# Kernel optimization log

Hardware: AMD Instinct MI355X
Metric: run time of the kernel (lower is better)

Reference implementation:

```python
import jax, jax.numpy as jnp
import numpy as np

EPS = 1e-8
N_ITER = 3
S = 8      # n_slots
D = 64     # slot_size
HID = 128  # mlp hidden


def _ln(x, w, b):
    m = jnp.mean(x, axis=-1, keepdims=True)
    v = jnp.var(x, axis=-1, keepdims=True)
    return (x - m) * jax.lax.rsqrt(v + 1e-5) * w + b


def setup_inputs() -> dict:
    key = jax.random.key(0)
    ks = jax.random.split(key, 20)
    B, N, Din = 128, 4096, 64
    g = lambda k, sh, s: (jax.random.normal(k, sh, jnp.float32) * s)
    return {
        "inputs": jax.random.normal(ks[0], (B, N, Din), jnp.float32),
        "eps_noise": jax.random.normal(ks[1], (B, S, D), jnp.float32),
        "slot_mu": g(ks[2], (1, 1, D), 0.1),
        "slot_logvar": g(ks[3], (1, 1, D), 0.1),
        "k_w": g(ks[4], (D, Din), 1.0 / np.sqrt(Din)),
        "v_w": g(ks[5], (D, Din), 1.0 / np.sqrt(Din)),
        "q_w": g(ks[6], (D, D), 1.0 / np.sqrt(D)),
        "ni_w": jnp.ones((Din,), jnp.float32), "ni_b": jnp.zeros((Din,), jnp.float32),
        "ns_w": jnp.ones((D,), jnp.float32),  "ns_b": jnp.zeros((D,), jnp.float32),
        "nr_w": jnp.ones((D,), jnp.float32),  "nr_b": jnp.zeros((D,), jnp.float32),
        "gru_wih": g(ks[7], (3 * D, D), 1.0 / np.sqrt(D)),
        "gru_whh": g(ks[8], (3 * D, D), 1.0 / np.sqrt(D)),
        "gru_bih": jnp.zeros((3 * D,), jnp.float32),
        "gru_bhh": jnp.zeros((3 * D,), jnp.float32),
        "mlp_w1": g(ks[9], (HID, D), 1.0 / np.sqrt(D)),
        "mlp_w2": g(ks[10], (D, HID), 1.0 / np.sqrt(HID)),
        "mlp_b2": jnp.zeros((D,), jnp.float32),
    }


def _gru(x, h, wih, whh, bih, bhh):
    gi = x @ wih.T + bih  # [BS, 3D]
    gh = h @ whh.T + bhh
    i_r, i_z, i_n = jnp.split(gi, 3, axis=-1)
    h_r, h_z, h_n = jnp.split(gh, 3, axis=-1)
    r = jax.nn.sigmoid(i_r + h_r)
    z = jax.nn.sigmoid(i_z + h_z)
    n = jnp.tanh(i_n + r * h_n)
    return (1.0 - z) * n + z * h


def _step(slots, k, v, q_w, ns_w, ns_b, nr_w, nr_b,
          gru_wih, gru_whh, gru_bih, gru_bhh, mlp_w1, mlp_w2, mlp_b2):
    B = slots.shape[0]
    q = _ln(slots, ns_w, ns_b) @ q_w.T                     # [B,S,D]
    logits = jnp.einsum('bnd,bsd->bns', k, q)              # [B,N,S]
    w = jax.nn.softmax(logits, axis=-1) + EPS              # softmax over slots
    w = w / jnp.sum(w, axis=-2, keepdims=True)             # renorm over tokens
    atten_maps = jnp.einsum('bns,bnd->bsd', w, v)          # [B,S,D]
    h = _gru(atten_maps.reshape(B * S, D), slots.reshape(B * S, D),
             gru_wih, gru_whh, gru_bih, gru_bhh)
    h = h + (jax.nn.relu(_ln(h, nr_w, nr_b) @ mlp_w1.T) @ mlp_w2.T + mlp_b2)
    return h.reshape(B, S, D), w


def reference(inputs, eps_noise, slot_mu, slot_logvar, k_w, v_w, q_w,
              ni_w, ni_b, ns_w, ns_b, nr_w, nr_b,
              gru_wih, gru_whh, gru_bih, gru_bhh, mlp_w1, mlp_w2, mlp_b2):
    std = jnp.exp(0.5 * slot_logvar)
    slots = slot_mu + std * eps_noise                      # [B,S,D]
    x = _ln(inputs, ni_w, ni_b)
    k = (x @ k_w.T) / np.sqrt(D).astype(np.float32)        # [B,N,D]
    v = x @ v_w.T
    args = (q_w, ns_w, ns_b, nr_w, nr_b, gru_wih, gru_whh,
            gru_bih, gru_bhh, mlp_w1, mlp_w2, mlp_b2)
    for _ in range(N_ITER):
        slots, w = _step(slots, k, v, *args)
    slots, w = _step(jax.lax.stop_gradient(slots), k, v, *args)
    return slots, w
```

## Files before the change

kernel.cpp:

```cpp
#include <hip/hip_runtime.h>
#include <hip/hip_bf16.h>

#define BB 128
#define NN 4096
#define DD 64
#define SS 8
#define HH 128

typedef __attribute__((ext_vector_type(8))) short short8;
typedef __attribute__((ext_vector_type(4))) float f32x4;

__device__ __forceinline__ float warp_red_sum(float v) {
    #pragma unroll
    for (int off = 32; off; off >>= 1) v += __shfl_xor(v, off);
    return v;
}

__device__ __forceinline__ float bcastlane(float v, int l) {
    return __int_as_float(__builtin_amdgcn_readlane(__float_as_int(v), l));
}

__device__ __forceinline__ unsigned short bfu(float f) {
    __hip_bfloat16 h = __float2bfloat16(f);
    return *(unsigned short*)&h;
}

__device__ __forceinline__ unsigned pk2(float a, float b) {
    return (unsigned)bfu(a) | ((unsigned)bfu(b) << 16);
}

__global__ __launch_bounds__(256) void prep_kernel(
    const float* __restrict__ k_w, const float* __restrict__ v_w, const float* __restrict__ q_w,
    const float* __restrict__ wih, const float* __restrict__ whh,
    const float* __restrict__ w1, const float* __restrict__ w2,
    unsigned short* __restrict__ wcat, float* __restrict__ qwT,
    float* __restrict__ wihT, float* __restrict__ whhT,
    float* __restrict__ w1T, float* __restrict__ w2T)
{
    int i0 = blockIdx.x * blockDim.x + threadIdx.x;
    int nthr = gridDim.x * blockDim.x;
    for (int t = i0; t < 8192; t += nthr) {
        int n = t >> 6, k = t & 63;
        float val = (n < 64) ? k_w[n * 64 + k] * 0.125f : v_w[(n - 64) * 64 + k];
        wcat[t] = bfu(val);
    }
    for (int t = i0; t < 4096; t += nthr) {
        int r = t >> 6, c = t & 63;
        qwT[t] = q_w[c * 64 + r];
    }
    for (int t = i0; t < 12288; t += nthr) {
        int r = t / 192, c = t % 192;
        wihT[t] = wih[c * 64 + r];
        whhT[t] = whh[c * 64 + r];
    }
    for (int t = i0; t < 8192; t += nthr) {
        int r = t >> 7, c = t & 127;
        w1T[t] = w1[c * 64 + r];
    }
    for (int t = i0; t < 8192; t += nthr) {
        int r = t >> 6, c = t & 63;
        w2T[t] = w2[c * 128 + r];
    }
}

__global__ __launch_bounds__(256) void slots_init_kernel(
    const float* __restrict__ eps, const float* __restrict__ mu,
    const float* __restrict__ lv, float* __restrict__ slots)
{
    int idx = blockIdx.x * blockDim.x + threadIdx.x;
    int d = idx & 63;
    slots[idx] = mu[d] + __expf(0.5f * lv[d]) * eps[idx];
}

__global__ __launch_bounds__(256) void phase_a_mfma(
    const float* __restrict__ inp, const unsigned short* __restrict__ wcat,
    const float* __restrict__ niw, const float* __restrict__ nib,
    unsigned short* __restrict__ kbu, unsigned short* __restrict__ vbt)
{
    __shared__ short smemA[18432];
    short* Xs = smemA;
    short* Ws = smemA + 9216;
    float* tbuf = (float*)smemA;
    const int tid = threadIdx.x, lane = tid & 63, widx = tid >> 6;

    {
        const unsigned* wg = (const unsigned*)wcat;
        #pragma unroll 4
        for (int t = tid; t < 4096; t += 256) {
            int n = t >> 5, kp = t & 31;
            *(unsigned*)&Ws[n * 72 + kp * 2] = wg[t];
        }
    }

    const int tg = lane >> 4, dq = lane & 15;
    const float4 wni = *(const float4*)&niw[dq * 4];
    const float4 bni = *(const float4*)&nib[dq * 4];
    const int tok0 = blockIdx.x * 128;
    #pragma unroll
    for (int it = 0; it < 8; ++it) {
        const int m = widx * 32 + it * 4 + tg;
        float4 x = *(const float4*)&inp[(size_t)(tok0 + m) * 64 + dq * 4];
        float s1 = x.x + x.y + x.z + x.w;
        float s2 = fmaf(x.x, x.x, fmaf(x.y, x.y, fmaf(x.z, x.z, x.w * x.w)));
        #pragma unroll
        for (int o = 1; o < 16; o <<= 1) { s1 += __shfl_xor(s1, o); s2 += __shfl_xor(s2, o); }
        float mean = s1 * (1.0f / 64.0f);
        float var = s2 * (1.0f / 64.0f) - mean * mean;
        float rstd = rsqrtf(var + 1e-5f);
        float y0 = (x.x - mean) * rstd * wni.x + bni.x;
        float y1 = (x.y - mean) * rstd * wni.y + bni.y;
        float y2 = (x.z - mean) * rstd * wni.z + bni.z;
        float y3 = (x.w - mean) * rstd * wni.w + bni.w;
        uint2 p; p.x = pk2(y0, y1); p.y = pk2(y2, y3);
        *(uint2*)&Xs[m * 72 + dq * 4] = p;
    }
    __syncthreads();

    const int quad = lane >> 4, l16 = lane & 15;
    short8 afr[2][2];
    #pragma unroll
    for (int mt = 0; mt < 2; ++mt)
        #pragma unroll
        for (int ks = 0; ks < 2; ++ks)
            afr[mt][ks] = *(const short8*)&Xs[(widx * 32 + mt * 16 + l16) * 72 + ks * 32 + quad * 8];

    f32x4 acc[2][8];
    #pragma unroll
    for (int mt = 0; mt < 2; ++mt)
        #pragma unroll
        for (int nt = 0; nt < 8; ++nt)
            acc[mt][nt] = (f32x4){0.f, 0.f, 0.f, 0.f};

    #pragma unroll
    for (int nt = 0; nt < 8; ++nt) {
        #pragma unroll
        for (int ks = 0; ks < 2; ++ks) {
            short8 bfr = *(const short8*)&Ws[(nt * 16 + l16) * 72 + ks * 32 + quad * 8];
            acc[0][nt] = __builtin_amdgcn_mfma_f32_16x16x32_bf16(afr[0][ks], bfr, acc[0][nt], 0, 0, 0);
            acc[1][nt] = __builtin_amdgcn_mfma_f32_16x16x32_bf16(afr[1][ks], bfr, acc[1][nt], 0, 0, 0);
        }
    }

    __syncthreads();
    #pragma unroll
    for (int mt = 0; mt < 2; ++mt)
        #pragma unroll
        for (int nt = 0; nt < 4; ++nt)
            #pragma unroll
            for (int r = 0; r < 4; ++r)
                tbuf[(widx * 32 + mt * 16 + quad * 4 + r) * 68 + nt * 16 + l16] = acc[mt][nt][r];
    __syncthreads();
    {
        const int row = tid >> 1, half = tid & 1;
        #pragma unroll
        for (int c = 0; c < 4; ++c) {
            float4 f0 = *(float4*)&tbuf[row * 68 + half * 32 + c * 8];
            float4 f1 = *(float4*)&tbuf[row * 68 + half * 32 + c * 8 + 4];
            uint4 o;
            o.x = pk2(f0.x, f0.y); o.y = pk2(f0.z, f0.w);
            o.z = pk2(f1.x, f1.y); o.w = pk2(f1.z, f1.w);
            *(uint4*)&kbu[(size_t)(tok0 + row) * 64 + half * 32 + c * 8] = o;
        }
    }

    __syncthreads();
    #pragma unroll
    for (int mt = 0; mt < 2; ++mt)
        #pragma unroll
        for (int nt = 4; nt < 8; ++nt)
            #pragma unroll
            for (int r = 0; r < 4; ++r)
                tbuf[((nt - 4) * 16 + l16) * 132 + widx * 32 + mt * 16 + quad * 4 + r] = acc[mt][nt][r];
    __syncthreads();
    {
        const int b = blockIdx.x >> 5, tin = (blockIdx.x & 31) * 128;
        const int d = tid >> 2, q4 = tid & 3;
        #pragma unroll
        for (int c = 0; c < 4; ++c) {
            float4 f0 = *(float4*)&tbuf[d * 132 + q4 * 32 + c * 8];
            float4 f1 = *(float4*)&tbuf[d * 132 + q4 * 32 + c * 8 + 4];
            uint4 o;
            o.x = pk2(f0.x, f0.y); o.y = pk2(f0.z, f0.w);
            o.z = pk2(f1.x, f1.y); o.w = pk2(f1.z, f1.w);
            *(uint4*)&vbt[((size_t)b * 64 + d) * 4096 + tin + q4 * 32 + c * 8] = o;
        }
    }
}

__global__ __launch_bounds__(256) void q_kernel(
    const float* __restrict__ slots, const float* __restrict__ qwT,
    const float* __restrict__ nsw, const float* __restrict__ nsb,
    unsigned short* __restrict__ qout)
{
    const int lane = threadIdx.x & 63;
    const int row = blockIdx.x * 4 + (threadIdx.x >> 6);
    float x = slots[row * 64 + lane];
    float m = warp_red_sum(x) * (1.0f / 64.0f);
    float dx = x - m;
    float var = warp_red_sum(dx * dx) * (1.0f / 64.0f);
    float xln = dx * rsqrtf(var + 1e-5f) * nsw[lane] + nsb[lane];
    float acc = 0.f;
    #pragma unroll 16
    for (int i = 0; i < 64; ++i) acc = fmaf(bcastlane(xln, i), qwT[i * 64 + lane], acc);
    qout[row * 64 + lane] = bfu(acc);
}

__global__ __launch_bounds__(256) void attn_mfma(
    const __hip_bfloat16* __restrict__ kb, const unsigned short* __restrict__ vbt,
    const unsigned short* __restrict__ qb,
    float* __restrict__ numer, float* __restrict__ denom, float* __restrict__ wout)
{
    __shared__ unsigned short smem[24192];
    unsigned short* Qs = smem;
    const int tid = threadIdx.x, lane = tid & 63, widx = tid >> 6;
    unsigned short* wls = smem + 1152 + widx * 1152;
    unsigned short* vt  = smem + 5760 + widx * 4608;
    const int b = blockIdx.y;

    for (int t = tid; t < 1024; t += 256) {
        int s = t >> 6, dd = t & 63;
        Qs[s * 72 + dd] = (s < 8) ? qb[b * 512 + t] : (unsigned short)0;
    }
    for (int t = lane; t < 576; t += 64) wls[576 + t] = 0;
    __syncthreads();

    const int quad = lane >> 4, l16 = lane & 15;
    short8 bq0 = *(const short8*)&Qs[l16 * 72 + quad * 8];
    short8 bq1 = *(const short8*)&Qs[l16 * 72 + 32 + quad * 8];

    f32x4 accv[4];
    #pragma unroll
    for (int nt = 0; nt < 4; ++nt) accv[nt] = (f32x4){0.f, 0.f, 0.f, 0.f};
    float dsum = 0.f;

    const int twave0 = blockIdx.x * 512 + widx * 128;
    const int vd = lane >> 3, vc = (lane & 7) * 8;
    #pragma unroll
    for (int iter = 0; iter < 2; ++iter) {
        const int t0 = twave0 + iter * 64;
        uint4 vld[8];
        #pragma unroll
        for (int i = 0; i < 8; ++i)
            vld[i] = *(const uint4*)&vbt[((size_t)b * 64 + i * 8 + vd) * 4096 + t0 + vc];

        #pragma unroll
        for (int t4 = 0; t4 < 4; ++t4) {
            const size_t krow = ((size_t)b * NN + t0 + t4 * 16 + l16) * 64;
            short8 ak0 = *(const short8*)&kb[krow + quad * 8];
            short8 ak1 = *(const short8*)&kb[krow + 32 + quad * 8];
            f32x4 lg = (f32x4){0.f, 0.f, 0.f, 0.f};
            lg = __builtin_amdgcn_mfma_f32_16x16x32_bf16(ak0, bq0, lg, 0, 0, 0);
            lg = __builtin_amdgcn_mfma_f32_16x16x32_bf16(ak1, bq1, lg, 0, 0, 0);
            float wv[4];
            #pragma unroll
            for (int r = 0; r < 4; ++r) {
                float e = __expf(lg[r]);
                float s = e;
                s += __shfl_xor(s, 1); s += __shfl_xor(s, 2); s += __shfl_xor(s, 4);
                wv[r] = e / s + 1e-8f;
                dsum += wv[r];
            }
            if (l16 < 8) {
                *(unsigned*)&wls[l16 * 72 + t4 * 16 + quad * 4]     = pk2(wv[0], wv[1]);
                *(unsigned*)&wls[l16 * 72 + t4 * 16 + quad * 4 + 2] = pk2(wv[2], wv[3]);
                if (wout) {
                    float* wp = wout + ((size_t)b * NN + t0 + t4 * 16 + quad * 4) * 8 + l16;
                    wp[0] = wv[0]; wp[8] = wv[1]; wp[16] = wv[2]; wp[24] = wv[3];
                }
            }
        }
        #pragma unroll
        for (int i = 0; i < 8; ++i)
            *(uint4*)&vt[(i * 8 + vd) * 72 + vc] = vld[i];
        #pragma unroll
        for (int ks = 0; ks < 2; ++ks) {
            short8 aw = *(const short8*)&wls[l16 * 72 + ks * 32 + quad * 8];
            #pragma unroll
            for (int nt = 0; nt < 4; ++nt) {
                short8 bv = *(const short8*)&vt[(nt * 16 + l16) * 72 + ks * 32 + quad * 8];
                accv[nt] = __builtin_amdgcn_mfma_f32_16x16x32_bf16(aw, bv, accv[nt], 0, 0, 0);
            }
        }
    }
    dsum += __shfl_xor(dsum, 16);
    dsum += __shfl_xor(dsum, 32);
    __syncthreads();
    float* red = (float*)(smem + 5760);
    float* dred = red + 2048;
    if (quad < 2) {
        #pragma unroll
        for (int nt = 0; nt < 4; ++nt)
            #pragma unroll
            for (int r = 0; r < 4; ++r)
                red[widx * 512 + (quad * 4 + r) * 64 + nt * 16 + l16] = accv[nt][r];
    }
    if (quad == 0 && l16 < 8) dred[widx * 8 + l16] = dsum;
    __syncthreads();
    for (int e = tid; e < 512; e += 256)
        atomicAdd(numer + (size_t)b * 512 + e, red[e] + red[512 + e] + red[1024 + e] + red[1536 + e]);
    if (tid < 8)
        atomicAdd(denom + b * 8 + tid, dred[tid] + dred[8 + tid] + dred[16 + tid] + dred[24 + tid]);
}

__global__ __launch_bounds__(256) void gru_kernel(
    const float* __restrict__ numer, const float* __restrict__ denom,
    const float* __restrict__ slotsIn,
    const float* __restrict__ wihT, const float* __restrict__ whhT,
    const float* __restrict__ w1T, const float* __restrict__ w2T,
    const float* __restrict__ bih, const float* __restrict__ bhh,
    const float* __restrict__ nrw, const float* __restrict__ nrb,
    const float* __restrict__ b2, float* __restrict__ slotsOut)
{
    const int lane = threadIdx.x & 63;
    const int row = blockIdx.x * 4 + (threadIdx.x >> 6);
    float x = numer[row * 64 + lane] / denom[row];
    float h = slotsIn[row * 64 + lane];
    float air = 0, aiz = 0, ain = 0, ahr = 0, ahz = 0, ahn = 0;
    #pragma unroll 8
    for (int i = 0; i < 64; ++i) {
        float xi = bcastlane(x, i), hi = bcastlane(h, i);
        const float* wi = wihT + i * 192;
        const float* wh = whhT + i * 192;
        air = fmaf(xi, wi[lane], air);
        aiz = fmaf(xi, wi[64 + lane], aiz);
        ain = fmaf(xi, wi[128 + lane], ain);
        ahr = fmaf(hi, wh[lane], ahr);
        ahz = fmaf(hi, wh[64 + lane], ahz);
        ahn = fmaf(hi, wh[128 + lane], ahn);
    }
    air += bih[lane]; aiz += bih[64 + lane]; ain += bih[128 + lane];
    ahr += bhh[lane]; ahz += bhh[64 + lane]; ahn += bhh[128 + lane];
    float r = 1.f / (1.f + __expf(-(air + ahr)));
    float z = 1.f / (1.f + __expf(-(aiz + ahz)));
    float n = tanhf(ain + r * ahn);
    float hn = (1.f - z) * n + z * h;
    float m = warp_red_sum(hn) * (1.0f / 64.0f);
    float dx = hn - m;
    float var = warp_red_sum(dx * dx) * (1.0f / 64.0f);
    float u = dx * rsqrtf(var + 1e-5f) * nrw[lane] + nrb[lane];
    float o0 = 0.f, o1 = 0.f;
    #pragma unroll 8
    for (int i = 0; i < 64; ++i) {
        float ui = bcastlane(u, i);
        const float* w1r = w1T + i * 128;
        o0 = fmaf(ui, w1r[lane], o0);
        o1 = fmaf(ui, w1r[64 + lane], o1);
    }
    o0 = fmaxf(o0, 0.f); o1 = fmaxf(o1, 0.f);
    float y = 0.f;
    #pragma unroll 8
    for (int j = 0; j < 64; ++j) y = fmaf(bcastlane(o0, j), w2T[j * 64 + lane], y);
    #pragma unroll 8
    for (int j = 0; j < 64; ++j) y = fmaf(bcastlane(o1, j), w2T[(64 + j) * 64 + lane], y);
    y += b2[lane];
    slotsOut[row * 64 + lane] = hn + y;
}

__global__ __launch_bounds__(256) void renorm_kernel(float* __restrict__ wout,
                                                     const float* __restrict__ denom)
{
    const size_t i4 = (size_t)blockIdx.x * blockDim.x + threadIdx.x;
    const size_t b = i4 >> 13;
    const int half = (int)(i4 & 1);
    float4 v = reinterpret_cast<float4*>(wout)[i4];
    const float4 dv = reinterpret_cast<const float4*>(denom)[b * 2 + half];
    v.x /= dv.x; v.y /= dv.y; v.z /= dv.z; v.w /= dv.w;
    reinterpret_cast<float4*>(wout)[i4] = v;
}

extern "C" void kernel_launch(void* const* d_in, const int* in_sizes, int n_in,
                              void* d_out, int out_size, void* d_ws, size_t ws_size,
                              hipStream_t stream)
{
    const float* inputs  = (const float*)d_in[0];
    const float* eps_n   = (const float*)d_in[1];
    const float* mu      = (const float*)d_in[2];
    const float* lv      = (const float*)d_in[3];
    const float* k_w     = (const float*)d_in[4];
    const float* v_w     = (const float*)d_in[5];
    const float* q_w     = (const float*)d_in[6];
    const float* ni_w    = (const float*)d_in[7];
    const float* ni_b    = (const float*)d_in[8];
    const float* ns_w    = (const float*)d_in[9];
    const float* ns_b    = (const float*)d_in[10];
    const float* nr_w    = (const float*)d_in[11];
    const float* nr_b    = (const float*)d_in[12];
    const float* gru_wih = (const float*)d_in[13];
    const float* gru_whh = (const float*)d_in[14];
    const float* gru_bih = (const float*)d_in[15];
    const float* gru_bhh = (const float*)d_in[16];
    const float* mlp_w1  = (const float*)d_in[17];
    const float* mlp_w2  = (const float*)d_in[18];
    const float* mlp_b2  = (const float*)d_in[19];

    char* wsb = (char*)d_ws;
    __hip_bfloat16* kb  = (__hip_bfloat16*)wsb;
    unsigned short* vbt = (unsigned short*)(wsb + 67108864);
    float* f      = (float*)(wsb + 134217728);
    float* slotsA = f;
    float* slotsB = f + 65536;
    unsigned short* qb = (unsigned short*)(f + 131072);
    float* numer  = f + 196608;
    float* denom  = f + 262144;
    unsigned short* wcat = (unsigned short*)(f + 263168);
    float* qwT    = f + 263168 + 4096;
    float* wihT   = qwT + 4096;
    float* whhT   = wihT + 12288;
    float* w1T    = whhT + 12288;
    float* w2T    = w1T + 8192;

    float* out_slots = (float*)d_out;
    float* out_w     = out_slots + 65536;

    prep_kernel<<<64, 256, 0, stream>>>(k_w, v_w, q_w, gru_wih, gru_whh, mlp_w1, mlp_w2,
                                        wcat, qwT, wihT, whhT, w1T, w2T);
    slots_init_kernel<<<256, 256, 0, stream>>>(eps_n, mu, lv, slotsA);
    phase_a_mfma<<<4096, 256, 0, stream>>>(inputs, wcat, ni_w, ni_b,
                                           (unsigned short*)kb, vbt);

    float* cur = slotsA;
    for (int step = 0; step < 4; ++step) {
        hipMemsetAsync(numer, 0, (65536 + 1024) * sizeof(float), stream);
        q_kernel<<<256, 256, 0, stream>>>(cur, qwT, ns_w, ns_b, qb);
        attn_mfma<<<dim3(8, 128), 256, 0, stream>>>(kb, vbt, qb, numer, denom,
                                                    step == 3 ? out_w : nullptr);
        float* nxt = (step == 3) ? out_slots : ((step & 1) ? slotsA : slotsB);
        gru_kernel<<<256, 256, 0, stream>>>(numer, denom, cur, wihT, whhT, w1T, w2T,
                                            gru_bih, gru_bhh, nr_w, nr_b, mlp_b2, nxt);
        cur = nxt;
    }
    renorm_kernel<<<4096, 256, 0, stream>>>(out_w, denom);
}
```

Before: 451.4 us.

## Fold K/V projections into per-slot query and output, drop K/V materialization

Rather than projecting every token into K and V, the attention kernel now runs on the layer-normed bf16 inputs directly. The query is pre-multiplied by k_w (q' = q·Wk/8), and the aggregated per-slot result is projected through v_w afterwards inside the GRU kernel. The separate q kernel and memset are fused into the GRU and init kernels, with numer/denom double-buffered and zeroed ahead of the next step. This removes the phase-A MFMA GEMM and several launches, at the cost of extra per-slot matvecs and slightly different bf16 rounding.

Measured after the change: 456.1 us. No clear change (+1.0%).

```diff
diff --git a/kernel.cpp b/kernel.cpp
--- a/kernel.cpp
+++ b/kernel.cpp
@@ -30,23 +30,19 @@
 }
 
 __global__ __launch_bounds__(256) void prep_kernel(
-    const float* __restrict__ k_w, const float* __restrict__ v_w, const float* __restrict__ q_w,
+    const float* __restrict__ v_w, const float* __restrict__ q_w,
     const float* __restrict__ wih, const float* __restrict__ whh,
     const float* __restrict__ w1, const float* __restrict__ w2,
-    unsigned short* __restrict__ wcat, float* __restrict__ qwT,
+    float* __restrict__ vwT, float* __restrict__ qwT,
     float* __restrict__ wihT, float* __restrict__ whhT,
     float* __restrict__ w1T, float* __restrict__ w2T)
 {
     int i0 = blockIdx.x * blockDim.x + threadIdx.x;
     int nthr = gridDim.x * blockDim.x;
-    for (int t = i0; t < 8192; t += nthr) {
-        int n = t >> 6, k = t & 63;
-        float val = (n < 64) ? k_w[n * 64 + k] * 0.125f : v_w[(n - 64) * 64 + k];
-        wcat[t] = bfu(val);
-    }
     for (int t = i0; t < 4096; t += nthr) {
-        int r = t >> 6, c = t & 63;
-        qwT[t] = q_w[c * 64 + r];
+        int i = t >> 6, o = t & 63;
+        vwT[t] = v_w[o * 64 + i];
+        qwT[t] = q_w[o * 64 + i];
     }
     for (int t = i0; t < 12288; t += nthr) {
         int r = t / 192, c = t % 192;
@@ -63,35 +59,40 @@
     }
 }
 
-__global__ __launch_bounds__(256) void slots_init_kernel(
+__global__ __launch_bounds__(256) void init_q_kernel(
     const float* __restrict__ eps, const float* __restrict__ mu,
-    const float* __restrict__ lv, float* __restrict__ slots)
-{
-    int idx = blockIdx.x * blockDim.x + threadIdx.x;
-    int d = idx & 63;
-    slots[idx] = mu[d] + __expf(0.5f * lv[d]) * eps[idx];
-}
-
-__global__ __launch_bounds__(256) void phase_a_mfma(
-    const float* __restrict__ inp, const unsigned short* __restrict__ wcat,
-    const float* __restrict__ niw, const float* __restrict__ nib,
-    unsigned short* __restrict__ kbu, unsigned short* __restrict__ vbt)
-{
-    __shared__ short smemA[18432];
-    short* Xs = smemA;
-    short* Ws = smemA + 9216;
-    float* tbuf = (float*)smemA;
+    const float* __restrict__ lv, const float* __restrict__ qwT,
+    const float* __restrict__ k_w,
+    const float* __restrict__ nsw, const float* __restrict__ nsb,
+    float* __restrict__ slots, unsigned short* __restrict__ qb,
+    float* __restrict__ zbuf)
+{
+    const int tid = threadIdx.x, lane = tid & 63;
+    const int row = blockIdx.x * 4 + (tid >> 6);
+    const int idx = row * 64 + lane;
+    float s0 = mu[lane] + __expf(0.5f * lv[lane]) * eps[idx];
+    slots[idx] = s0;
+    float m = warp_red_sum(s0) * (1.0f / 64.0f);
+    float dx = s0 - m;
+    float var = warp_red_sum(dx * dx) * (1.0f / 64.0f);
+    float xln = dx * rsqrtf(var + 1e-5f) * nsw[lane] + nsb[lane];
+    float q = 0.f;
+    #pragma unroll 8
+    for (int i = 0; i < 64; ++i) q = fmaf(bcastlane(xln, i), qwT[i * 64 + lane], q);
+    float qp = 0.f;
+    #pragma unroll 8
+    for (int o = 0; o < 64; ++o) qp = fmaf(bcastlane(q, o), k_w[o * 64 + lane], qp);
+    qb[idx] = bfu(qp * 0.125f);
+    int g = blockIdx.x * 256 + tid;
+    for (int j = g; j < 66560; j += 65536) zbuf[j] = 0.f;
+}
+
+__global__ __launch_bounds__(256) void phase_a_ln(
+    const float* __restrict__ inp, const float* __restrict__ niw, const float* __restrict__ nib,
+    unsigned short* __restrict__ xb, unsigned short* __restrict__ xbt)
+{
+    __shared__ unsigned short xt[64 * 136];
     const int tid = threadIdx.x, lane = tid & 63, widx = tid >> 6;
-
-    {
-        const unsigned* wg = (const unsigned*)wcat;
-        #pragma unroll 4
-        for (int t = tid; t < 4096; t += 256) {
-            int n = t >> 5, kp = t & 31;
-            *(unsigned*)&Ws[n * 72 + kp * 2] = wg[t];
-        }
-    }
-
     const int tg = lane >> 4, dq = lane & 15;
     const float4 wni = *(const float4*)&niw[dq * 4];
     const float4 bni = *(const float4*)&nib[dq * 4];
@@ -112,101 +113,24 @@
         float y2 = (x.z - mean) * rstd * wni.z + bni.z;
         float y3 = (x.w - mean) * rstd * wni.w + bni.w;
         uint2 p; p.x = pk2(y0, y1); p.y = pk2(y2, y3);
-        *(uint2*)&Xs[m * 72 + dq * 4] = p;
+        *(uint2*)&xb[(size_t)(tok0 + m) * 64 + dq * 4] = p;
+        xt[(dq * 4 + 0) * 136 + m] = bfu(y0);
+        xt[(dq * 4 + 1) * 136 + m] = bfu(y1);
+        xt[(dq * 4 + 2) * 136 + m] = bfu(y2);
+        xt[(dq * 4 + 3) * 136 + m] = bfu(y3);
     }
     __syncthreads();
-
-    const int quad = lane >> 4, l16 = lane & 15;
-    short8 afr[2][2];
-    #pragma unroll
-    for (int mt = 0; mt < 2; ++mt)
-        #pragma unroll
-        for (int ks = 0; ks < 2; ++ks)
-            afr[mt][ks] = *(const short8*)&Xs[(widx * 32 + mt * 16 + l16) * 72 + ks * 32 + quad * 8];
-
-    f32x4 acc[2][8];
-    #pragma unroll
-    for (int mt = 0; mt < 2; ++mt)
-        #pragma unroll
-        for (int nt = 0; nt < 8; ++nt)
-            acc[mt][nt] = (f32x4){0.f, 0.f, 0.f, 0.f};
-
-    #pragma unroll
-    for (int nt = 0; nt < 8; ++nt) {
-        #pragma unroll
-        for (int ks = 0; ks < 2; ++ks) {
-            short8 bfr = *(const short8*)&Ws[(nt * 16 + l16) * 72 + ks * 32 + quad * 8];
-            acc[0][nt] = __builtin_amdgcn_mfma_f32_16x16x32_bf16(afr[0][ks], bfr, acc[0][nt], 0, 0, 0);
-            acc[1][nt] = __builtin_amdgcn_mfma_f32_16x16x32_bf16(afr[1][ks], bfr, acc[1][nt], 0, 0, 0);
-        }
-    }
-
-    __syncthreads();
-    #pragma unroll
-    for (int mt = 0; mt < 2; ++mt)
-        #pragma unroll
-        for (int nt = 0; nt < 4; ++nt)
-            #pragma unroll
-            for (int r = 0; r < 4; ++r)
-                tbuf[(widx * 32 + mt * 16 + quad * 4 + r) * 68 + nt * 16 + l16] = acc[mt][nt][r];
-    __syncthreads();
-    {
-        const int row = tid >> 1, half = tid & 1;
-        #pragma unroll
-        for (int c = 0; c < 4; ++c) {
-            float4 f0 = *(float4*)&tbuf[row * 68 + half * 32 + c * 8];
-            float4 f1 = *(float4*)&tbuf[row * 68 + half * 32 + c * 8 + 4];
-            uint4 o;
-            o.x = pk2(f0.x, f0.y); o.y = pk2(f0.z, f0.w);
-            o.z = pk2(f1.x, f1.y); o.w = pk2(f1.z, f1.w);
-            *(uint4*)&kbu[(size_t)(tok0 + row) * 64 + half * 32 + c * 8] = o;
-        }
-    }
-
-    __syncthreads();
-    #pragma unroll
-    for (int mt = 0; mt < 2; ++mt)
-        #pragma unroll
-        for (int nt = 4; nt < 8; ++nt)
-            #pragma unroll
-            for (int r = 0; r < 4; ++r)
-                tbuf[((nt - 4) * 16 + l16) * 132 + widx * 32 + mt * 16 + quad * 4 + r] = acc[mt][nt][r];
-    __syncthreads();
-    {
-        const int b = blockIdx.x >> 5, tin = (blockIdx.x & 31) * 128;
-        const int d = tid >> 2, q4 = tid & 3;
-        #pragma unroll
-        for (int c = 0; c < 4; ++c) {
-            float4 f0 = *(float4*)&tbuf[d * 132 + q4 * 32 + c * 8];
-            float4 f1 = *(float4*)&tbuf[d * 132 + q4 * 32 + c * 8 + 4];
-            uint4 o;
-            o.x = pk2(f0.x, f0.y); o.y = pk2(f0.z, f0.w);
-            o.z = pk2(f1.x, f1.y); o.w = pk2(f1.z, f1.w);
-            *(uint4*)&vbt[((size_t)b * 64 + d) * 4096 + tin + q4 * 32 + c * 8] = o;
-        }
-    }
-}
-
-__global__ __launch_bounds__(256) void q_kernel(
-    const float* __restrict__ slots, const float* __restrict__ qwT,
-    const float* __restrict__ nsw, const float* __restrict__ nsb,
-    unsigned short* __restrict__ qout)
-{
-    const int lane = threadIdx.x & 63;
-    const int row = blockIdx.x * 4 + (threadIdx.x >> 6);
-    float x = slots[row * 64 + lane];
-    float m = warp_red_sum(x) * (1.0f / 64.0f);
-    float dx = x - m;
-    float var = warp_red_sum(dx * dx) * (1.0f / 64.0f);
-    float xln = dx * rsqrtf(var + 1e-5f) * nsw[lane] + nsb[lane];
-    float acc = 0.f;
-    #pragma unroll 16
-    for (int i = 0; i < 64; ++i) acc = fmaf(bcastlane(xln, i), qwT[i * 64 + lane], acc);
-    qout[row * 64 + lane] = bfu(acc);
+    const int b = blockIdx.x >> 5, tin = (blockIdx.x & 31) * 128;
+    const int d = tid >> 2, q4 = tid & 3;
+    #pragma unroll
+    for (int c = 0; c < 4; ++c) {
+        uint4 o = *(uint4*)&xt[d * 136 + q4 * 32 + c * 8];
+        *(uint4*)&xbt[((size_t)b * 64 + d) * 4096 + tin + q4 * 32 + c * 8] = o;
+    }
 }
 
 __global__ __launch_bounds__(256) void attn_mfma(
-    const __hip_bfloat16* __restrict__ kb, const unsigned short* __restrict__ vbt,
+    const __hip_bfloat16* __restrict__ xb, const unsigned short* __restrict__ xbt,
     const unsigned short* __restrict__ qb,
     float* __restrict__ numer, float* __restrict__ denom, float* __restrict__ wout)
 {
@@ -241,13 +165,13 @@
         uint4 vld[8];
         #pragma unroll
         for (int i = 0; i < 8; ++i)
-            vld[i] = *(const uint4*)&vbt[((size_t)b * 64 + i * 8 + vd) * 4096 + t0 + vc];
+            vld[i] = *(const uint4*)&xbt[((size_t)b * 64 + i * 8 + vd) * 4096 + t0 + vc];
 
         #pragma unroll
         for (int t4 = 0; t4 < 4; ++t4) {
             const size_t krow = ((size_t)b * NN + t0 + t4 * 16 + l16) * 64;
-            short8 ak0 = *(const short8*)&kb[krow + quad * 8];
-            short8 ak1 = *(const short8*)&kb[krow + 32 + quad * 8];
+            short8 ak0 = *(const short8*)&xb[krow + quad * 8];
+            short8 ak1 = *(const short8*)&xb[krow + 32 + quad * 8];
             f32x4 lg = (f32x4){0.f, 0.f, 0.f, 0.f};
             lg = __builtin_amdgcn_mfma_f32_16x16x32_bf16(ak0, bq0, lg, 0, 0, 0);
             lg = __builtin_amdgcn_mfma_f32_16x16x32_bf16(ak1, bq1, lg, 0, 0, 0);
@@ -302,18 +226,26 @@
         atomicAdd(denom + b * 8 + tid, dred[tid] + dred[8 + tid] + dred[16 + tid] + dred[24 + tid]);
 }
 
-__global__ __launch_bounds__(256) void gru_kernel(
-    const float* __restrict__ numer, const float* __restrict__ denom,
+__global__ __launch_bounds__(256) void gru_q_kernel(
+    const float* __restrict__ numerX, const float* __restrict__ denom,
     const float* __restrict__ slotsIn,
-    const float* __restrict__ wihT, const float* __restrict__ whhT,
+    const float* __restrict__ vwT, const float* __restrict__ wihT, const float* __restrict__ whhT,
     const float* __restrict__ w1T, const float* __restrict__ w2T,
     const float* __restrict__ bih, const float* __restrict__ bhh,
     const float* __restrict__ nrw, const float* __restrict__ nrb,
-    const float* __restrict__ b2, float* __restrict__ slotsOut)
-{
-    const int lane = threadIdx.x & 63;
-    const int row = blockIdx.x * 4 + (threadIdx.x >> 6);
-    float x = numer[row * 64 + lane] / denom[row];
+    const float* __restrict__ b2,
+    const float* __restrict__ qwT, const float* __restrict__ k_w,
+    const float* __restrict__ nsw, const float* __restrict__ nsb,
+    float* __restrict__ slotsOut, unsigned short* __restrict__ qb,
+    float* __restrict__ zbuf)
+{
+    const int tid = threadIdx.x, lane = tid & 63;
+    const int row = blockIdx.x * 4 + (tid >> 6);
+    float nx = numerX[row * 64 + lane];
+    float xp = 0.f;
+    #pragma unroll 8
+    for (int i = 0; i < 64; ++i) xp = fmaf(bcastlane(nx, i), vwT[i * 64 + lane], xp);
+    float x = xp / denom[row];
     float h = slotsIn[row * 64 + lane];
     float air = 0, aiz = 0, ain = 0, ahr = 0, ahz = 0, ahn = 0;
     #pragma unroll 8
@@ -353,7 +285,21 @@
     #pragma unroll 8
     for (int j = 0; j < 64; ++j) y = fmaf(bcastlane(o1, j), w2T[(64 + j) * 64 + lane], y);
     y += b2[lane];
-    slotsOut[row * 64 + lane] = hn + y;
+    float out = hn + y;
+    slotsOut[row * 64 + lane] = out;
+    float m2 = warp_red_sum(out) * (1.0f / 64.0f);
+    float dx2 = out - m2;
+    float var2 = warp_red_sum(dx2 * dx2) * (1.0f / 64.0f);
+    float u2 = dx2 * rsqrtf(var2 + 1e-5f) * nsw[lane] + nsb[lane];
+    float q = 0.f;
+    #pragma unroll 8
+    for (int i = 0; i < 64; ++i) q = fmaf(bcastlane(u2, i), qwT[i * 64 + lane], q);
+    float qp = 0.f;
+    #pragma unroll 8
+    for (int o = 0; o < 64; ++o) qp = fmaf(bcastlane(q, o), k_w[o * 64 + lane], qp);
+    qb[row * 64 + lane] = bfu(qp * 0.125f);
+    int g = blockIdx.x * 256 + tid;
+    for (int j = g; j < 66560; j += 65536) zbuf[j] = 0.f;
 }
 
 __global__ __launch_bounds__(256) void renorm_kernel(float* __restrict__ wout,
@@ -394,40 +340,47 @@
     const float* mlp_b2  = (const float*)d_in[19];
 
     char* wsb = (char*)d_ws;
-    __hip_bfloat16* kb  = (__hip_bfloat16*)wsb;
-    unsigned short* vbt = (unsigned short*)(wsb + 67108864);
+    unsigned short* xb  = (unsigned short*)wsb;
+    unsigned short* xbt = (unsigned short*)(wsb + 67108864);
     float* f      = (float*)(wsb + 134217728);
     float* slotsA = f;
     float* slotsB = f + 65536;
     unsigned short* qb = (unsigned short*)(f + 131072);
-    float* numer  = f + 196608;
-    float* denom  = f + 262144;
-    unsigned short* wcat = (unsigned short*)(f + 263168);
-    float* qwT    = f + 263168 + 4096;
-    float* wihT   = qwT + 4096;
-    float* whhT   = wihT + 12288;
-    float* w1T    = whhT + 12288;
-    float* w2T    = w1T + 8192;
+    float* numer0 = f + 163840;
+    float* denom0 = f + 229376;
+    float* numer1 = f + 230400;
+    float* denom1 = f + 295936;
+    float* vwT    = f + 296960;
+    float* qwT    = f + 301056;
+    float* wihT   = f + 305152;
+    float* whhT   = f + 317440;
+    float* w1T    = f + 329728;
+    float* w2T    = f + 337920;
 
     float* out_slots = (float*)d_out;
     float* out_w     = out_slots + 65536;
 
-    prep_kernel<<<64, 256, 0, stream>>>(k_w, v_w, q_w, gru_wih, gru_whh, mlp_w1, mlp_w2,
-                                        wcat, qwT, wihT, whhT, w1T, w2T);
-    slots_init_kernel<<<256, 256, 0, stream>>>(eps_n, mu, lv, slotsA);
-    phase_a_mfma<<<4096, 256, 0, stream>>>(inputs, wcat, ni_w, ni_b,
-                                           (unsigned short*)kb, vbt);
+    prep_kernel<<<64, 256, 0, stream>>>(v_w, q_w, gru_wih, gru_whh, mlp_w1, mlp_w2,
+                                        vwT, qwT, wihT, whhT, w1T, w2T);
+    init_q_kernel<<<256, 256, 0, stream>>>(eps_n, mu, lv, qwT, k_w, ns_w, ns_b,
+                                           slotsA, qb, numer0);
+    phase_a_ln<<<4096, 256, 0, stream>>>(inputs, ni_w, ni_b, xb, xbt);
 
     float* cur = slotsA;
+    float* numers[2] = {numer0, numer1};
+    float* denoms[2] = {denom0, denom1};
     for (int step = 0; step < 4; ++step) {
-        hipMemsetAsync(numer, 0, (65536 + 1024) * sizeof(float), stream);
-        q_kernel<<<256, 256, 0, stream>>>(cur, qwT, ns_w, ns_b, qb);
-        attn_mfma<<<dim3(8, 128), 256, 0, stream>>>(kb, vbt, qb, numer, denom,
+        int pb = step & 1;
+        attn_mfma<<<dim3(8, 128), 256, 0, stream>>>((const __hip_bfloat16*)xb, xbt, qb,
+                                                    numers[pb], denoms[pb],
                                                     step == 3 ? out_w : nullptr);
         float* nxt = (step == 3) ? out_slots : ((step & 1) ? slotsA : slotsB);
-        gru_kernel<<<256, 256, 0, stream>>>(numer, denom, cur, wihT, whhT, w1T, w2T,
-                                            gru_bih, gru_bhh, nr_w, nr_b, mlp_b2, nxt);
+        gru_q_kernel<<<256, 256, 0, stream>>>(numers[pb], denoms[pb], cur,
+                                              vwT, wihT, whhT, w1T, w2T,
+                                              gru_bih, gru_bhh, nr_w, nr_b, mlp_b2,
+                                              qwT, k_w, ns_w, ns_b,
+                                              nxt, qb, numers[1 - pb]);
         cur = nxt;
     }
-    renorm_kernel<<<4096, 256, 0, stream>>>(out_w, denom);
-}
+    renorm_kernel<<<4096, 256, 0, stream>>>(out_w, denom1);
+}
```
